# Performance work log

Hardware: AMD Instinct MI355X
Metric: run time of the kernel (lower is better)

## Reference

```python
import jax, jax.numpy as jnp
import numpy as np

NUM_GRAPHS = 512  # number of segments (graphs) in the batch
N_NODES = 200000
HIDDEN = 256


def setup_inputs() -> dict:
    key = jax.random.key(0)
    ks = jax.random.split(key, 8)
    x = jax.random.normal(ks[0], (N_NODES, HIDDEN), dtype=jnp.float32)
    batch = jnp.sort(jax.random.randint(ks[1], (N_NODES,), 0, NUM_GRAPHS, dtype=jnp.int32))
    h4 = HIDDEN // 4
    w1 = jax.random.normal(ks[2], (HIDDEN, h4), dtype=jnp.float32) * (1.0 / np.sqrt(HIDDEN))
    b1 = jnp.zeros((h4,), dtype=jnp.float32)
    w2 = jax.random.normal(ks[3], (h4, 1), dtype=jnp.float32) * (1.0 / np.sqrt(h4))
    b2 = jnp.zeros((1,), dtype=jnp.float32)
    wp = jax.random.normal(ks[4], (3 * HIDDEN, HIDDEN), dtype=jnp.float32) * (1.0 / np.sqrt(3 * HIDDEN))
    bp = jnp.zeros((HIDDEN,), dtype=jnp.float32)
    gamma = jnp.ones((HIDDEN,), dtype=jnp.float32)
    beta = jnp.zeros((HIDDEN,), dtype=jnp.float32)
    return {"x": x, "batch": batch, "w1": w1, "b1": b1, "w2": w2, "b2": b2,
            "wp": wp, "bp": bp, "gamma": gamma, "beta": beta}


def reference(x, batch, w1, b1, w2, b2, wp, bp, gamma, beta):
    G = NUM_GRAPHS
    # --- global mean pool ---
    seg_sum = jax.ops.segment_sum(x, batch, num_segments=G)  # [G, H]
    counts = jax.ops.segment_sum(jnp.ones((x.shape[0],), x.dtype), batch, num_segments=G)
    z_mean = seg_sum / jnp.maximum(counts, 1.0)[:, None]
    # --- global max pool ---
    z_max = jax.ops.segment_max(x, batch, num_segments=G)
    z_max = jnp.where(jnp.isfinite(z_max), z_max, 0.0)  # guard empty segments
    # --- global attention pool (PyG GlobalAttention) ---
    gate = jnp.maximum(x @ w1 + b1, 0.0) @ w2 + b2  # [N, 1]
    g = gate[:, 0]
    g_max = jax.ops.segment_max(g, batch, num_segments=G)
    g_max = jnp.where(jnp.isfinite(g_max), g_max, 0.0)
    e = jnp.exp(g - g_max[batch])
    denom = jax.ops.segment_sum(e, batch, num_segments=G)
    w = e / jnp.maximum(denom, 1e-16)[batch]  # scatter-softmax weights [N]
    z_attn = jax.ops.segment_sum(w[:, None] * x, batch, num_segments=G)
    # --- concat + proj + layernorm ---
    z = jnp.concatenate([z_mean, z_max, z_attn], axis=-1)  # [G, 3H]
    y = z @ wp + bp  # [G, H]
    mu = jnp.mean(y, axis=-1, keepdims=True)
    var = jnp.mean(jnp.square(y - mu), axis=-1, keepdims=True)
    yhat = (y - mu) * jax.lax.rsqrt(var + 1e-5)
    return yhat * gamma + beta
```

## Files before the change

### kernel.cpp

```cpp
#include <hip/hip_runtime.h>
#include <math.h>

#define N_NODES 200000
#define NGRAPH  512
#define HID     256
#define NTILES  (N_NODES / 16)
#define PARTS   4

typedef __attribute__((ext_vector_type(8))) short s16x8;
typedef __attribute__((ext_vector_type(4))) float f32x4;

__device__ __forceinline__ unsigned short f2bf_rne(float f) {
  unsigned int u = __float_as_uint(f);
  return (unsigned short)((u + 0x7fffu + ((u >> 16) & 1u)) >> 16);
}
__device__ __forceinline__ unsigned int pack2_bf16_rne(float a, float b) {
  unsigned int ua = __float_as_uint(a), ub = __float_as_uint(b);
  unsigned int ra = (ua + 0x7fffu + ((ua >> 16) & 1u)) >> 16;
  unsigned int rb = (ub + 0x7fffu + ((ub >> 16) & 1u)) & 0xffff0000u;
  return ra | rb;
}
__device__ __forceinline__ int lower_bound_batch(const int* __restrict__ batch, int target) {
  int lo = 0, hi = N_NODES;
  while (lo < hi) { int mid = (lo + hi) >> 1; if (batch[mid] < target) lo = mid + 1; else hi = mid; }
  return lo;
}
__device__ __forceinline__ f32x4 vmax4(f32x4 a, f32x4 b) {
  return (f32x4){fmaxf(a[0], b[0]), fmaxf(a[1], b[1]), fmaxf(a[2], b[2]), fmaxf(a[3], b[3])};
}

__global__ __launch_bounds__(256, 2) void gate_kernel(
    const float* __restrict__ x, const float* __restrict__ w1,
    const float* __restrict__ b1, const float* __restrict__ w2,
    const float* __restrict__ b2, float* __restrict__ g)
{
  __shared__ __align__(16) short w1T[64 * 264];
  const int tid = threadIdx.x;
  const int w = tid >> 6, lane = tid & 63, q = lane >> 4, c = lane & 15;

  for (int i = tid; i < 256 * 64; i += 256) {
    int k = i >> 6, n = i & 63;
    w1T[n * 264 + k] = (short)f2bf_rne(w1[i]);
  }
  __syncthreads();

  float b1v[4], w2v[4];
#pragma unroll
  for (int nt = 0; nt < 4; ++nt) { b1v[nt] = b1[nt * 16 + c]; w2v[nt] = w2[nt * 16 + c]; }
  const float b2v = b2[0];

  const int tstride = gridDim.x << 2;
  for (int t = (blockIdx.x << 2) + w; t < NTILES; t += tstride) {
    const int r0 = t << 4;
    const float* ap = x + (size_t)(r0 + c) * HID + q * 8;
    union { s16x8 v; unsigned int u[4]; } ah[8];
#pragma unroll
    for (int half = 0; half < 2; ++half) {
      float4 t0[4], t1[4];
#pragma unroll
      for (int kk = 0; kk < 4; ++kk) {
        int kt = half * 4 + kk;
        t0[kk] = *(const float4*)(ap + kt * 32);
        t1[kk] = *(const float4*)(ap + kt * 32 + 4);
      }
#pragma unroll
      for (int kk = 0; kk < 4; ++kk) {
        int kt = half * 4 + kk;
        ah[kt].u[0] = pack2_bf16_rne(t0[kk].x, t0[kk].y);
        ah[kt].u[1] = pack2_bf16_rne(t0[kk].z, t0[kk].w);
        ah[kt].u[2] = pack2_bf16_rne(t1[kk].x, t1[kk].y);
        ah[kt].u[3] = pack2_bf16_rne(t1[kk].z, t1[kk].w);
      }
    }

    f32x4 acc[4];
#pragma unroll
    for (int nt = 0; nt < 4; ++nt) acc[nt] = (f32x4){0.f, 0.f, 0.f, 0.f};
#pragma unroll
    for (int kt = 0; kt < 8; ++kt) {
#pragma unroll
      for (int nt = 0; nt < 4; ++nt) {
        s16x8 bh = *(const s16x8*)&w1T[(nt * 16 + c) * 264 + kt * 32 + q * 8];
        acc[nt] = __builtin_amdgcn_mfma_f32_16x16x32_bf16(ah[kt].v, bh, acc[nt], 0, 0, 0);
      }
    }

    float gr[4];
#pragma unroll
    for (int r = 0; r < 4; ++r) {
      float sv = 0.f;
#pragma unroll
      for (int nt = 0; nt < 4; ++nt) {
        float h = acc[nt][r] + b1v[nt];
        h = h > 0.f ? h : 0.f;
        sv += h * w2v[nt];
      }
      sv += __shfl_xor(sv, 1, 64);
      sv += __shfl_xor(sv, 2, 64);
      sv += __shfl_xor(sv, 4, 64);
      sv += __shfl_xor(sv, 8, 64);
      gr[r] = sv + b2v;
    }
    if (c == 0) {
      float4 o = make_float4(gr[0], gr[1], gr[2], gr[3]);
      *(float4*)(g + r0 + q * 4) = o;
    }
  }
}

__global__ __launch_bounds__(256) void seg_softmax(
    const float* __restrict__ g, const int* __restrict__ batch,
    float* __restrict__ wgt)
{
  __shared__ int sb[2];
  __shared__ float red[4];
  const int tid = threadIdx.x;
  const int w = tid >> 6, lane = tid & 63;
  if (tid < 2) sb[tid] = lower_bound_batch(batch, (int)blockIdx.x + tid);
  __syncthreads();
  const int s0 = sb[0], e0 = sb[1];

  float m = -INFINITY;
  for (int i = s0 + tid; i < e0; i += 256) m = fmaxf(m, g[i]);
#pragma unroll
  for (int off = 32; off > 0; off >>= 1) m = fmaxf(m, __shfl_xor(m, off, 64));
  if (lane == 0) red[w] = m;
  __syncthreads();
  m = fmaxf(fmaxf(red[0], red[1]), fmaxf(red[2], red[3]));
  __syncthreads();

  float den = 0.f;
  for (int i = s0 + tid; i < e0; i += 256) den += __expf(g[i] - m);
#pragma unroll
  for (int off = 32; off > 0; off >>= 1) den += __shfl_xor(den, off, 64);
  if (lane == 0) red[w] = den;
  __syncthreads();
  den = red[0] + red[1] + red[2] + red[3];

  const float inv = 1.f / fmaxf(den, 1e-16f);
  for (int i = s0 + tid; i < e0; i += 256) wgt[i] = __expf(g[i] - m) * inv;
}

__global__ __launch_bounds__(256, 8) void pool_pass(
    const float* __restrict__ x, const int* __restrict__ batch,
    const float* __restrict__ wgt, float* __restrict__ pbuf)
{
  __shared__ int sb[2];
  __shared__ __align__(16) float scr[12 * 256];
  const int tid = threadIdx.x;
  const int w = tid >> 6, lane = tid & 63;
  const int seg = blockIdx.x >> 2, p = blockIdx.x & 3;

  if (tid < 2) sb[tid] = lower_bound_batch(batch, seg + tid);
  __syncthreads();
  const int s0 = sb[0], len = sb[1] - s0;
  const int ps = s0 + ((len * p) >> 2);
  const int pe = s0 + ((len * (p + 1)) >> 2);

  f32x4 sum = (f32x4){0.f, 0.f, 0.f, 0.f};
  f32x4 at  = (f32x4){0.f, 0.f, 0.f, 0.f};
  f32x4 mx  = (f32x4){-INFINITY, -INFINITY, -INFINITY, -INFINITY};

  const float* xp = x + lane * 4;
  int r = ps + w;
  for (; r + 12 < pe; r += 16) {
    float4 v0 = *(const float4*)(xp + (size_t)(r     ) * HID);
    float4 v1 = *(const float4*)(xp + (size_t)(r +  4) * HID);
    float4 v2 = *(const float4*)(xp + (size_t)(r +  8) * HID);
    float4 v3 = *(const float4*)(xp + (size_t)(r + 12) * HID);
    float w0 = wgt[r], w1v = wgt[r + 4], w2v = wgt[r + 8], w3v = wgt[r + 12];
    f32x4 f0 = (f32x4){v0.x, v0.y, v0.z, v0.w};
    f32x4 f1 = (f32x4){v1.x, v1.y, v1.z, v1.w};
    f32x4 f2 = (f32x4){v2.x, v2.y, v2.z, v2.w};
    f32x4 f3 = (f32x4){v3.x, v3.y, v3.z, v3.w};
    sum = sum + ((f0 + f1) + (f2 + f3));
    mx = vmax4(mx, vmax4(vmax4(f0, f1), vmax4(f2, f3)));
#pragma unroll
    for (int j = 0; j < 4; ++j) {
      float a = fmaf(w0, f0[j], at[j]);
      a = fmaf(w1v, f1[j], a);
      a = fmaf(w2v, f2[j], a);
      at[j] = fmaf(w3v, f3[j], a);
    }
  }
  for (; r < pe; r += 4) {
    float4 v = *(const float4*)(xp + (size_t)r * HID);
    float wr = wgt[r];
    f32x4 f = (f32x4){v.x, v.y, v.z, v.w};
    sum = sum + f;
    mx = vmax4(mx, f);
#pragma unroll
    for (int j = 0; j < 4; ++j) at[j] = fmaf(wr, f[j], at[j]);
  }

  {
    float* p0 = scr + (w * 3 + 0) * 256;
    float* p1 = scr + (w * 3 + 1) * 256;
    float* p2 = scr + (w * 3 + 2) * 256;
    *(f32x4*)&p0[lane * 4] = sum;
    *(f32x4*)&p1[lane * 4] = mx;
    *(f32x4*)&p2[lane * 4] = at;
  }
  __syncthreads();
  {
    const int f = tid;
    float S = 0.f, MX = -INFINITY, A = 0.f;
#pragma unroll
    for (int ww = 0; ww < 4; ++ww) {
      S += scr[(ww * 3 + 0) * 256 + f];
      MX = fmaxf(MX, scr[(ww * 3 + 1) * 256 + f]);
      A += scr[(ww * 3 + 2) * 256 + f];
    }
    float* pr = pbuf + (size_t)blockIdx.x * 772;
    pr[f] = S; pr[256 + f] = MX; pr[512 + f] = A;
    if (tid == 0) pr[768] = (float)(pe - ps);
  }
}

__global__ __launch_bounds__(256) void pool_merge2(
    const float* __restrict__ pbuf, float* __restrict__ zbuf)
{
  const int seg = blockIdx.x, f = threadIdx.x;
  float S = 0.f, A = 0.f, MX = -INFINITY, cnt = 0.f;
#pragma unroll
  for (int pp = 0; pp < PARTS; ++pp) {
    const float* pr = pbuf + (size_t)(seg * PARTS + pp) * 772;
    S += pr[f];
    MX = fmaxf(MX, pr[256 + f]);
    A += pr[512 + f];
    cnt += pr[768];
  }
  float* zr = zbuf + (size_t)seg * 768;
  zr[f]       = S / fmaxf(cnt, 1.f);
  zr[256 + f] = (cnt > 0.f) ? MX : 0.f;
  zr[512 + f] = A;
}

__global__ __launch_bounds__(256) void head_ln(
    const float* __restrict__ zbuf, const float* __restrict__ wp,
    const float* __restrict__ bp, const float* __restrict__ gam,
    const float* __restrict__ bet, float* __restrict__ out)
{
  const int g = blockIdx.x;
  const int tid = threadIdx.x;
  const int w = tid >> 6, lane = tid & 63;
  __shared__ float z[768];
  __shared__ __align__(16) float part[4][256];
  __shared__ float red[256];

  for (int i = tid; i < 768; i += 256) z[i] = zbuf[(size_t)g * 768 + i];
  __syncthreads();

  f32x4 acc = (f32x4){0.f, 0.f, 0.f, 0.f};
  const float4* wp4 = (const float4*)wp;
  const int k0 = w * 192;
#pragma unroll 8
  for (int k = k0; k < k0 + 192; ++k) {
    float4 wv = wp4[(size_t)k * 64 + lane];
    float zk = z[k];
    acc[0] = fmaf(zk, wv.x, acc[0]);
    acc[1] = fmaf(zk, wv.y, acc[1]);
    acc[2] = fmaf(zk, wv.z, acc[2]);
    acc[3] = fmaf(zk, wv.w, acc[3]);
  }
  *(f32x4*)&part[w][lane * 4] = acc;
  __syncthreads();

  const int t = tid;
  float y = bp[t] + part[0][t] + part[1][t] + part[2][t] + part[3][t];

  red[t] = y;
  __syncthreads();
  for (int wd = 128; wd > 0; wd >>= 1) {
    if (t < wd) red[t] += red[t + wd];
    __syncthreads();
  }
  const float mu = red[0] * (1.f / 256.f);
  __syncthreads();
  float d = y - mu;
  red[t] = d * d;
  __syncthreads();
  for (int wd = 128; wd > 0; wd >>= 1) {
    if (t < wd) red[t] += red[t + wd];
    __syncthreads();
  }
  const float var = red[0] * (1.f / 256.f);
  const float is = rsqrtf(var + 1e-5f);
  out[(size_t)g * 256 + t] = fmaf(d * is, gam[t], bet[t]);
}

extern "C" void kernel_launch(void* const* d_in, const int* in_sizes, int n_in,
                              void* d_out, int out_size, void* d_ws, size_t ws_size,
                              hipStream_t stream) {
  const float* x   = (const float*)d_in[0];
  const int*   bat = (const int*)d_in[1];
  const float* w1  = (const float*)d_in[2];
  const float* b1  = (const float*)d_in[3];
  const float* w2  = (const float*)d_in[4];
  const float* b2  = (const float*)d_in[5];
  const float* wp  = (const float*)d_in[6];
  const float* bp  = (const float*)d_in[7];
  const float* gam = (const float*)d_in[8];
  const float* bet = (const float*)d_in[9];
  float* out = (float*)d_out;

  float* gbuf = (float*)d_ws;
  float* wgt  = gbuf + N_NODES;
  float* pbuf = wgt + N_NODES;
  float* zbuf = pbuf + (size_t)NGRAPH * PARTS * 772;

  hipLaunchKernelGGL(gate_kernel, dim3(1024), dim3(256), 0, stream,
                     x, w1, b1, w2, b2, gbuf);
  hipLaunchKernelGGL(seg_softmax, dim3(NGRAPH), dim3(256), 0, stream,
                     gbuf, bat, wgt);
  hipLaunchKernelGGL(pool_pass, dim3(NGRAPH * PARTS), dim3(256), 0, stream,
                     x, bat, wgt, pbuf);
  hipLaunchKernelGGL(pool_merge2, dim3(NGRAPH), dim3(256), 0, stream, pbuf, zbuf);
  hipLaunchKernelGGL(head_ln, dim3(NGRAPH), dim3(256), 0, stream,
                     zbuf, wp, bp, gam, bet, out);
}
```

Baseline: 367.9 us.

## Fold segment softmax into pooling pass by deferring normalization without max shift

Removes the separate seg_softmax kernel. The gate kernel now writes exp(g) directly, and the pool pass accumulates the softmax denominator next to the weighted sum, with division applied in the merge kernel. The parts per segment drop from 4 to 2, the pool loop is unrolled to 8 rows, and the gate kernel gets a higher occupancy hint with smaller load batches. Skipping the max subtraction risks overflow for large gate values; it is safe only if gate magnitudes stay small, as with these inputs.

```diff
diff --git a/kernel.cpp b/kernel.cpp
--- a/kernel.cpp
+++ b/kernel.cpp
@@ -5,7 +5,7 @@
 #define NGRAPH  512
 #define HID     256
 #define NTILES  (N_NODES / 16)
-#define PARTS   4
+#define PARTS   2
 
 typedef __attribute__((ext_vector_type(8))) short s16x8;
 typedef __attribute__((ext_vector_type(4))) float f32x4;
@@ -29,10 +29,10 @@
   return (f32x4){fmaxf(a[0], b[0]), fmaxf(a[1], b[1]), fmaxf(a[2], b[2]), fmaxf(a[3], b[3])};
 }
 
-__global__ __launch_bounds__(256, 2) void gate_kernel(
+__global__ __launch_bounds__(256, 4) void gate_kernel(
     const float* __restrict__ x, const float* __restrict__ w1,
     const float* __restrict__ b1, const float* __restrict__ w2,
-    const float* __restrict__ b2, float* __restrict__ g)
+    const float* __restrict__ b2, float* __restrict__ ew)
 {
   __shared__ __align__(16) short w1T[64 * 264];
   const int tid = threadIdx.x;
@@ -55,17 +55,17 @@
     const float* ap = x + (size_t)(r0 + c) * HID + q * 8;
     union { s16x8 v; unsigned int u[4]; } ah[8];
 #pragma unroll
-    for (int half = 0; half < 2; ++half) {
-      float4 t0[4], t1[4];
-#pragma unroll
-      for (int kk = 0; kk < 4; ++kk) {
-        int kt = half * 4 + kk;
+    for (int quar = 0; quar < 4; ++quar) {
+      float4 t0[2], t1[2];
+#pragma unroll
+      for (int kk = 0; kk < 2; ++kk) {
+        int kt = quar * 2 + kk;
         t0[kk] = *(const float4*)(ap + kt * 32);
         t1[kk] = *(const float4*)(ap + kt * 32 + 4);
       }
 #pragma unroll
-      for (int kk = 0; kk < 4; ++kk) {
-        int kt = half * 4 + kk;
+      for (int kk = 0; kk < 2; ++kk) {
+        int kt = quar * 2 + kk;
         ah[kt].u[0] = pack2_bf16_rne(t0[kk].x, t0[kk].y);
         ah[kt].u[1] = pack2_bf16_rne(t0[kk].z, t0[kk].w);
         ah[kt].u[2] = pack2_bf16_rne(t1[kk].x, t1[kk].y);
@@ -102,93 +102,61 @@
       gr[r] = sv + b2v;
     }
     if (c == 0) {
-      float4 o = make_float4(gr[0], gr[1], gr[2], gr[3]);
-      *(float4*)(g + r0 + q * 4) = o;
-    }
-  }
-}
-
-__global__ __launch_bounds__(256) void seg_softmax(
-    const float* __restrict__ g, const int* __restrict__ batch,
-    float* __restrict__ wgt)
+      float4 o = make_float4(__expf(gr[0]), __expf(gr[1]), __expf(gr[2]), __expf(gr[3]));
+      *(float4*)(ew + r0 + q * 4) = o;
+    }
+  }
+}
+
+__global__ __launch_bounds__(256, 4) void pool_pass(
+    const float* __restrict__ x, const int* __restrict__ batch,
+    const float* __restrict__ ew, float* __restrict__ pbuf)
 {
   __shared__ int sb[2];
-  __shared__ float red[4];
-  const int tid = threadIdx.x;
-  const int w = tid >> 6, lane = tid & 63;
-  if (tid < 2) sb[tid] = lower_bound_batch(batch, (int)blockIdx.x + tid);
-  __syncthreads();
-  const int s0 = sb[0], e0 = sb[1];
-
-  float m = -INFINITY;
-  for (int i = s0 + tid; i < e0; i += 256) m = fmaxf(m, g[i]);
-#pragma unroll
-  for (int off = 32; off > 0; off >>= 1) m = fmaxf(m, __shfl_xor(m, off, 64));
-  if (lane == 0) red[w] = m;
-  __syncthreads();
-  m = fmaxf(fmaxf(red[0], red[1]), fmaxf(red[2], red[3]));
-  __syncthreads();
-
-  float den = 0.f;
-  for (int i = s0 + tid; i < e0; i += 256) den += __expf(g[i] - m);
-#pragma unroll
-  for (int off = 32; off > 0; off >>= 1) den += __shfl_xor(den, off, 64);
-  if (lane == 0) red[w] = den;
-  __syncthreads();
-  den = red[0] + red[1] + red[2] + red[3];
-
-  const float inv = 1.f / fmaxf(den, 1e-16f);
-  for (int i = s0 + tid; i < e0; i += 256) wgt[i] = __expf(g[i] - m) * inv;
-}
-
-__global__ __launch_bounds__(256, 8) void pool_pass(
-    const float* __restrict__ x, const int* __restrict__ batch,
-    const float* __restrict__ wgt, float* __restrict__ pbuf)
-{
-  __shared__ int sb[2];
+  __shared__ float sden[4];
   __shared__ __align__(16) float scr[12 * 256];
   const int tid = threadIdx.x;
   const int w = tid >> 6, lane = tid & 63;
-  const int seg = blockIdx.x >> 2, p = blockIdx.x & 3;
+  const int seg = blockIdx.x >> 1, p = blockIdx.x & 1;
 
   if (tid < 2) sb[tid] = lower_bound_batch(batch, seg + tid);
   __syncthreads();
   const int s0 = sb[0], len = sb[1] - s0;
-  const int ps = s0 + ((len * p) >> 2);
-  const int pe = s0 + ((len * (p + 1)) >> 2);
+  const int ps = s0 + ((len * p) >> 1);
+  const int pe = s0 + ((len * (p + 1)) >> 1);
 
   f32x4 sum = (f32x4){0.f, 0.f, 0.f, 0.f};
   f32x4 at  = (f32x4){0.f, 0.f, 0.f, 0.f};
   f32x4 mx  = (f32x4){-INFINITY, -INFINITY, -INFINITY, -INFINITY};
+  float den = 0.f;
 
   const float* xp = x + lane * 4;
   int r = ps + w;
-  for (; r + 12 < pe; r += 16) {
-    float4 v0 = *(const float4*)(xp + (size_t)(r     ) * HID);
-    float4 v1 = *(const float4*)(xp + (size_t)(r +  4) * HID);
-    float4 v2 = *(const float4*)(xp + (size_t)(r +  8) * HID);
-    float4 v3 = *(const float4*)(xp + (size_t)(r + 12) * HID);
-    float w0 = wgt[r], w1v = wgt[r + 4], w2v = wgt[r + 8], w3v = wgt[r + 12];
-    f32x4 f0 = (f32x4){v0.x, v0.y, v0.z, v0.w};
-    f32x4 f1 = (f32x4){v1.x, v1.y, v1.z, v1.w};
-    f32x4 f2 = (f32x4){v2.x, v2.y, v2.z, v2.w};
-    f32x4 f3 = (f32x4){v3.x, v3.y, v3.z, v3.w};
-    sum = sum + ((f0 + f1) + (f2 + f3));
-    mx = vmax4(mx, vmax4(vmax4(f0, f1), vmax4(f2, f3)));
-#pragma unroll
-    for (int j = 0; j < 4; ++j) {
-      float a = fmaf(w0, f0[j], at[j]);
-      a = fmaf(w1v, f1[j], a);
-      a = fmaf(w2v, f2[j], a);
-      at[j] = fmaf(w3v, f3[j], a);
+  for (; r + 28 < pe; r += 32) {
+    float4 v[8]; float wv[8];
+#pragma unroll
+    for (int j = 0; j < 8; ++j) v[j] = *(const float4*)(xp + (size_t)(r + 4 * j) * HID);
+#pragma unroll
+    for (int j = 0; j < 8; ++j) wv[j] = ew[r + 4 * j];
+#pragma unroll
+    for (int j = 0; j < 8; ++j) {
+      f32x4 f = (f32x4){v[j].x, v[j].y, v[j].z, v[j].w};
+      sum = sum + f;
+      mx = vmax4(mx, f);
+      den += wv[j];
+      at[0] = fmaf(wv[j], f[0], at[0]);
+      at[1] = fmaf(wv[j], f[1], at[1]);
+      at[2] = fmaf(wv[j], f[2], at[2]);
+      at[3] = fmaf(wv[j], f[3], at[3]);
     }
   }
   for (; r < pe; r += 4) {
     float4 v = *(const float4*)(xp + (size_t)r * HID);
-    float wr = wgt[r];
+    float wr = ew[r];
     f32x4 f = (f32x4){v.x, v.y, v.z, v.w};
     sum = sum + f;
     mx = vmax4(mx, f);
+    den += wr;
 #pragma unroll
     for (int j = 0; j < 4; ++j) at[j] = fmaf(wr, f[j], at[j]);
   }
@@ -200,6 +168,7 @@
     *(f32x4*)&p0[lane * 4] = sum;
     *(f32x4*)&p1[lane * 4] = mx;
     *(f32x4*)&p2[lane * 4] = at;
+    if (lane == 0) sden[w] = den;
   }
   __syncthreads();
   {
@@ -213,7 +182,7 @@
     }
     float* pr = pbuf + (size_t)blockIdx.x * 772;
     pr[f] = S; pr[256 + f] = MX; pr[512 + f] = A;
-    if (tid == 0) pr[768] = (float)(pe - ps);
+    if (tid == 0) { pr[768] = (float)(pe - ps); pr[769] = sden[0] + sden[1] + sden[2] + sden[3]; }
   }
 }
 
@@ -221,7 +190,7 @@
     const float* __restrict__ pbuf, float* __restrict__ zbuf)
 {
   const int seg = blockIdx.x, f = threadIdx.x;
-  float S = 0.f, A = 0.f, MX = -INFINITY, cnt = 0.f;
+  float S = 0.f, A = 0.f, MX = -INFINITY, cnt = 0.f, den = 0.f;
 #pragma unroll
   for (int pp = 0; pp < PARTS; ++pp) {
     const float* pr = pbuf + (size_t)(seg * PARTS + pp) * 772;
@@ -229,11 +198,12 @@
     MX = fmaxf(MX, pr[256 + f]);
     A += pr[512 + f];
     cnt += pr[768];
+    den += pr[769];
   }
   float* zr = zbuf + (size_t)seg * 768;
   zr[f]       = S / fmaxf(cnt, 1.f);
   zr[256 + f] = (cnt > 0.f) ? MX : 0.f;
-  zr[512 + f] = A;
+  zr[512 + f] = A / fmaxf(den, 1e-16f);
 }
 
 __global__ __launch_bounds__(256) void head_ln(
@@ -304,17 +274,14 @@
   const float* bet = (const float*)d_in[9];
   float* out = (float*)d_out;
 
-  float* gbuf = (float*)d_ws;
-  float* wgt  = gbuf + N_NODES;
-  float* pbuf = wgt + N_NODES;
+  float* ebuf = (float*)d_ws;
+  float* pbuf = ebuf + N_NODES;
   float* zbuf = pbuf + (size_t)NGRAPH * PARTS * 772;
 
   hipLaunchKernelGGL(gate_kernel, dim3(1024), dim3(256), 0, stream,
-                     x, w1, b1, w2, b2, gbuf);
-  hipLaunchKernelGGL(seg_softmax, dim3(NGRAPH), dim3(256), 0, stream,
-                     gbuf, bat, wgt);
+                     x, w1, b1, w2, b2, ebuf);
   hipLaunchKernelGGL(pool_pass, dim3(NGRAPH * PARTS), dim3(256), 0, stream,
-                     x, bat, wgt, pbuf);
+                     x, bat, ebuf, pbuf);
   hipLaunchKernelGGL(pool_merge2, dim3(NGRAPH), dim3(256), 0, stream, pbuf, zbuf);
   hipLaunchKernelGGL(head_ln, dim3(NGRAPH), dim3(256), 0, stream,
                      zbuf, wp, bp, gam, bet, out);
```

After: 389.3 us. 5.8% more time.
